# Kernel optimization log

Measured on AMD Instinct MI355X. Metric: run time of the kernel, lower is better.

## Reference

```python
import jax, jax.numpy as jnp
import numpy as np

N = 50000
E = 800000
D = 128
H = 8
HD = D // H


def setup_inputs() -> dict:
    key = jax.random.key(0)
    ks = jax.random.split(key, 12)
    s = 1.0 / np.sqrt(D)
    x = jax.random.normal(ks[0], (N, D), dtype=jnp.float32)
    edge_index = jax.random.randint(ks[1], (2, E), 0, N, dtype=jnp.int64)
    edge_bias = jax.random.normal(ks[2], (E, H), dtype=jnp.float32)
    Wq = jax.random.uniform(ks[3], (D, D), jnp.float32, -s, s)
    bq = jax.random.uniform(ks[4], (D,), jnp.float32, -s, s)
    Wk = jax.random.uniform(ks[5], (D, D), jnp.float32, -s, s)
    bk = jax.random.uniform(ks[6], (D,), jnp.float32, -s, s)
    Wv = jax.random.uniform(ks[7], (D, D), jnp.float32, -s, s)
    bv = jax.random.uniform(ks[8], (D,), jnp.float32, -s, s)
    Wo = jax.random.uniform(ks[9], (D, D), jnp.float32, -s, s)
    bo = jax.random.uniform(ks[10], (D,), jnp.float32, -s, s)
    return {"x": x, "edge_index": edge_index, "edge_bias": edge_bias,
            "Wq": Wq, "bq": bq, "Wk": Wk, "bk": bk,
            "Wv": Wv, "bv": bv, "Wo": Wo, "bo": bo}


def reference(x, edge_index, edge_bias, Wq, bq, Wk, bk, Wv, bv, Wo, bo):
    scale = HD ** -0.5
    row, col = edge_index[0], edge_index[1]
    # Node-level projections -> [N, H, HD]
    q = (x @ Wq + bq).reshape(N, H, HD)
    k = (x @ Wk + bk).reshape(N, H, HD)
    v = (x @ Wv + bv).reshape(N, H, HD)
    # Edge-level gather + per-edge attention logits [E, H]
    q_i = q[col]
    k_j = k[row]
    v_j = v[row]
    attn = jnp.einsum('ehd,ehd->eh', q_i, k_j) * scale + edge_bias
    # Scatter-softmax over incoming edges of each destination node (col)
    seg_max = jax.ops.segment_max(attn, col, num_segments=N)  # [N, H]
    seg_max = jnp.where(jnp.isfinite(seg_max), seg_max, 0.0)  # empty segments -> 0
    ex = jnp.exp(attn - seg_max[col])
    denom = jax.ops.segment_sum(ex, col, num_segments=N)      # [N, H]
    attn = ex / (denom[col] + 1e-16)
    # Scatter-add weighted values -> [N, H, HD]
    weighted_v = attn[:, :, None] * v_j
    out = jax.ops.segment_sum(weighted_v, col, num_segments=N)
    out = out.reshape(N, D)
    return out @ Wo + bo
```

## Files before the change

kernel.cpp:

```cpp
#include <hip/hip_runtime.h>
#include <math.h>

#define NN 50000
#define EE 800000
#define DD 128
#define HH 8
#define HDD 16
#define CAP 64
#define NXCD 8
#define NPG 6250
#define SL 2048
#define NSL 391
#define NSTRIP 3125
#define QB 782
#define FILLB 3128
#define LTS 130

typedef __attribute__((ext_vector_type(8))) short short8;
typedef __attribute__((ext_vector_type(4))) float f32x4;

union U8 { ushort u[8]; int4 v; short8 s; };

__device__ __forceinline__ ushort f2bf(float f) {
    uint u = __float_as_uint(f);
    uint r = (u + 0x7fffu + ((u >> 16) & 1u)) >> 16;
    return (ushort)r;
}
__device__ __forceinline__ float bf2f(ushort u) {
    return __uint_as_float(((uint)u) << 16);
}

__global__ void k_prep(const float* __restrict__ Wq, const float* __restrict__ Wk,
                       const float* __restrict__ Wv, const float* __restrict__ Wo,
                       const float* __restrict__ bq, const float* __restrict__ bk,
                       const float* __restrict__ bv, const float* __restrict__ bo,
                       ushort* __restrict__ Wt, float* __restrict__ bpack) {
    int tid = blockIdx.x * 256 + threadIdx.x;
    int w = tid >> 14, rem = tid & 16383, c = rem >> 7, i = rem & 127;
    const float* W = (w == 0) ? Wq : (w == 1) ? Wk : (w == 2) ? Wv : Wo;
    float s = (w == 0) ? 0.25f : 1.0f;
    Wt[(size_t)w * 16384 + c * 128 + i] = f2bf(W[i * 128 + c] * s);
    if (i == 0) {
        const float* B = (w == 0) ? bq : (w == 1) ? bk : (w == 2) ? bv : bo;
        bpack[w * 128 + c] = B[c] * s;
    }
}

__global__ __launch_bounds__(256) void k_pre(
    const float* __restrict__ x, const ushort* __restrict__ Wt,
    const float* __restrict__ bpk,
    ushort* __restrict__ qb, ushort* __restrict__ kk, ushort* __restrict__ vv,
    const int* __restrict__ col, const int* __restrict__ row,
    int* __restrict__ cursor, int2* __restrict__ reB) {
    __shared__ ushort T[4][16 * LTS];
    int tid = threadIdx.x;
    int b = blockIdx.x;

    if (b >= QB) {
        int fi = b - QB;
        int g = b & 7;
        int j = fi >> 3;
        int lo = g * NPG, hi = lo + NPG;
        int base = j * SL + tid * 8;
        if (base < EE) {
            int4 c0 = *(const int4*)&col[base];
            int4 c1 = *(const int4*)&col[base + 4];
            int cs[8] = {c0.x, c0.y, c0.z, c0.w, c1.x, c1.y, c1.z, c1.w};
            int lim = EE - base;
#pragma unroll
            for (int t = 0; t < 8; t++) {
                if (t < lim) {
                    int c = cs[t];
                    if (c >= lo && c < hi) {
                        int e = base + t;
                        int p = atomicAdd(&cursor[c], 1);
                        if (p < CAP) reB[(size_t)c * CAP + p] = make_int2(row[e], e);
                    }
                }
            }
        }
        return;
    }

    int wave = tid >> 6, lane = tid & 63;
    int strip = b * 4 + wave;
    if (strip >= NSTRIP) return;
    int r0 = strip * 16;
    int lr = lane & 15, lg = lane >> 4;
    ushort* Tw = T[wave];

    short8 afr[4];
    const float* xp = x + (size_t)(r0 + lr) * 128;
#pragma unroll
    for (int ks = 0; ks < 4; ks++) {
        const float* ap = xp + ks * 32 + lg * 8;
        float4 f0 = *(const float4*)ap;
        float4 f1 = *(const float4*)(ap + 4);
        U8 r;
        r.u[0] = f2bf(f0.x); r.u[1] = f2bf(f0.y); r.u[2] = f2bf(f0.z); r.u[3] = f2bf(f0.w);
        r.u[4] = f2bf(f1.x); r.u[5] = f2bf(f1.y); r.u[6] = f2bf(f1.z); r.u[7] = f2bf(f1.w);
        afr[ks] = r.s;
    }

    for (int w = 0; w < 3; w++) {
        f32x4 acc[8];
#pragma unroll
        for (int n = 0; n < 8; n++) acc[n] = (f32x4){0.f, 0.f, 0.f, 0.f};
        const ushort* Wb = Wt + (size_t)w * 16384;
#pragma unroll
        for (int ks = 0; ks < 4; ks++) {
            short8 bfr[8];
#pragma unroll
            for (int n = 0; n < 8; n++)
                bfr[n] = *(const short8*)&Wb[(n * 16 + lr) * 128 + ks * 32 + lg * 8];
#pragma unroll
            for (int n = 0; n < 8; n++)
                acc[n] = __builtin_amdgcn_mfma_f32_16x16x32_bf16(afr[ks], bfr[n], acc[n], 0, 0, 0);
        }

#pragma unroll
        for (int n = 0; n < 8; n++) {
            float bv_ = bpk[w * 128 + n * 16 + lr];
#pragma unroll
            for (int rg = 0; rg < 4; rg++)
                Tw[(lg * 4 + rg) * LTS + n * 16 + lr] = f2bf(acc[n][rg] + bv_);
        }
        ushort* dst = (w == 0) ? qb : (w == 1) ? kk : vv;
#pragma unroll
        for (int i = 0; i < 4; i++) {
            int4 vd = *(const int4*)&Tw[(i * 4 + lg) * LTS + lr * 8];
            *(int4*)&dst[(size_t)(r0 + i * 4 + lg) * 128 + lr * 8] = vd;
        }
    }
}

__global__ __launch_bounds__(256) void k_gemm_out(
    const ushort* __restrict__ A, const ushort* __restrict__ Bt,
    const float* __restrict__ bias, float* __restrict__ Cf) {
    int tid = threadIdx.x;
    int wave = tid >> 6, lane = tid & 63;
    int strip = blockIdx.x * 4 + wave;
    if (strip >= NSTRIP) return;
    int r0 = strip * 16;
    int lr = lane & 15, lg = lane >> 4;

    short8 afr[4];
#pragma unroll
    for (int ks = 0; ks < 4; ks++)
        afr[ks] = *(const short8*)&A[(size_t)(r0 + lr) * 128 + ks * 32 + lg * 8];

    f32x4 acc[8];
#pragma unroll
    for (int n = 0; n < 8; n++) acc[n] = (f32x4){0.f, 0.f, 0.f, 0.f};
#pragma unroll
    for (int ks = 0; ks < 4; ks++) {
        short8 bfr[8];
#pragma unroll
        for (int n = 0; n < 8; n++)
            bfr[n] = *(const short8*)&Bt[(n * 16 + lr) * 128 + ks * 32 + lg * 8];
#pragma unroll
        for (int n = 0; n < 8; n++)
            acc[n] = __builtin_amdgcn_mfma_f32_16x16x32_bf16(afr[ks], bfr[n], acc[n], 0, 0, 0);
    }
#pragma unroll
    for (int n = 0; n < 8; n++) {
        int gcol = n * 16 + lr;
        float bv_ = bias[gcol];
#pragma unroll
        for (int rg = 0; rg < 4; rg++) {
            int grow = r0 + lg * 4 + rg;
            Cf[(size_t)grow * 128 + gcol] = acc[n][rg] + bv_;
        }
    }
}

__global__ __launch_bounds__(256) void k_attn(
    const ushort* __restrict__ qb, const ushort* __restrict__ kk,
    const ushort* __restrict__ vv, const float* __restrict__ ebias,
    const int2* __restrict__ reB, const int* __restrict__ deg,
    ushort* __restrict__ aggb) {
    int wave = threadIdx.x >> 6;
    int lane = threadIdx.x & 63;
    int n = blockIdx.x * 4 + wave;
    if (n >= NN) return;
    int cnt = min(deg[n], CAP);
    const int2* bucket = reB + (size_t)n * CAP;
    int h = lane >> 3;
    int j = lane & 7;
    int hb = lane & ~7;

    float qf[16];
    {
        U8 q0, q1;
        const ushort* qp = qb + (size_t)n * DD + h * HDD;
        q0.v = *(const int4*)qp;
        q1.v = *(const int4*)(qp + 8);
#pragma unroll
        for (int t = 0; t < 8; t++) qf[t] = bf2f(q0.u[t]);
#pragma unroll
        for (int t = 0; t < 8; t++) qf[8 + t] = bf2f(q1.u[t]);
    }

    float m = -INFINITY;
    float denom = 0.f;
    float acc0 = 0.f, acc1 = 0.f;

    for (int idx = 0; idx < cnt; idx += 8) {
        int my = idx + j;
        bool valid = my < cnt;
        int2 re = valid ? bucket[my] : make_int2(0, 0);
        int r = re.x;
        float logit = -INFINITY;
        if (valid) {
            const ushort* kp = kk + (size_t)r * DD + h * HDD;
            U8 a0, a1;
            a0.v = *(const int4*)kp;
            a1.v = *(const int4*)(kp + 8);
            float d = 0.f;
#pragma unroll
            for (int t = 0; t < 8; t++) d += qf[t] * bf2f(a0.u[t]);
#pragma unroll
            for (int t = 0; t < 8; t++) d += qf[8 + t] * bf2f(a1.u[t]);
            logit = d + ebias[(size_t)re.y * HH + h];
        }
        float cm = logit;
        cm = fmaxf(cm, __shfl_xor(cm, 1));
        cm = fmaxf(cm, __shfl_xor(cm, 2));
        cm = fmaxf(cm, __shfl_xor(cm, 4));
        float mnew = fmaxf(m, cm);
        float sc = __expf(m - mnew);
        float p = __expf(logit - mnew);
        m = mnew;
        float ps = p;
        ps += __shfl_xor(ps, 1);
        ps += __shfl_xor(ps, 2);
        ps += __shfl_xor(ps, 4);
        denom = denom * sc + ps;
        acc0 *= sc;
        acc1 *= sc;
#pragma unroll
        for (int j2 = 0; j2 < 8; j2++) {
            float pj = __shfl(p, hb + j2);
            int rj = __shfl(r, hb + j2);
            uint vp = *(const uint*)(vv + (size_t)rj * DD + 2 * lane);
            acc0 += pj * bf2f((ushort)(vp & 0xffffu));
            acc1 += pj * bf2f((ushort)(vp >> 16));
        }
    }
    float inv = 1.0f / (denom + 1e-16f);
    uint pack = (uint)f2bf(acc0 * inv) | ((uint)f2bf(acc1 * inv) << 16);
    *(uint*)&aggb[(size_t)n * DD + 2 * lane] = pack;
}

extern "C" void kernel_launch(void* const* d_in, const int* in_sizes, int n_in,
                              void* d_out, int out_size, void* d_ws, size_t ws_size,
                              hipStream_t stream) {
    const float* x     = (const float*)d_in[0];
    const int*   eidx  = (const int*)d_in[1];
    const float* ebias = (const float*)d_in[2];
    const float* Wq    = (const float*)d_in[3];
    const float* bq    = (const float*)d_in[4];
    const float* Wk    = (const float*)d_in[5];
    const float* bk    = (const float*)d_in[6];
    const float* Wv    = (const float*)d_in[7];
    const float* bv    = (const float*)d_in[8];
    const float* Wo    = (const float*)d_in[9];
    const float* bo    = (const float*)d_in[10];
    float* out = (float*)d_out;

    const int* row = eidx;
    const int* col = eidx + EE;

    char* p = (char*)d_ws;
    ushort* qb    = (ushort*)p;  p += (size_t)NN * DD * 2;
    ushort* kk    = (ushort*)p;  p += (size_t)NN * DD * 2;
    ushort* vvp   = (ushort*)p;  p += (size_t)NN * DD * 2;
    ushort* aggb  = (ushort*)p;  p += (size_t)NN * DD * 2;
    ushort* Wt    = (ushort*)p;  p += (size_t)4 * 16384 * 2;
    float*  bpk   = (float*)p;   p += 4 * 128 * 4;
    int2*   reB   = (int2*)p;    p += (size_t)NN * CAP * 8;
    int* cursor   = (int*)p;     p += (size_t)NN * 4;

    hipMemsetAsync(cursor, 0, (size_t)NN * sizeof(int), stream);

    hipLaunchKernelGGL(k_prep, dim3(256), dim3(256), 0, stream,
                       Wq, Wk, Wv, Wo, bq, bk, bv, bo, Wt, bpk);

    hipLaunchKernelGGL(k_pre, dim3(QB + FILLB), dim3(256), 0, stream,
                       x, Wt, bpk, qb, kk, vvp, col, row, cursor, reB);

    hipLaunchKernelGGL(k_attn, dim3(NN / 4), dim3(256), 0, stream,
                       qb, kk, vvp, ebias, reB, cursor, aggb);

    hipLaunchKernelGGL(k_gemm_out, dim3((NSTRIP + 3) / 4), dim3(256), 0, stream,
                       aggb, Wt + 3 * 16384, bpk + 3 * 128, out);
}
```

Before: 178.1 us.

## Split CSR fill into two node halves and overlap with QKV and attention

Result: slower. 205.8 us (+15.5%).

```diff
diff --git a/kernel.cpp b/kernel.cpp
--- a/kernel.cpp
+++ b/kernel.cpp
@@ -7,13 +7,15 @@
 #define HH 8
 #define HDD 16
 #define CAP 64
-#define NXCD 8
-#define NPG 6250
+#define HALF 25000
+#define NPG 3125
 #define SL 2048
-#define NSL 391
 #define NSTRIP 3125
 #define QB 782
-#define FILLB 3128
+#define P1B 3910
+#define P2B 9380
+#define P3B 6250
+#define P4B 782
 #define LTS 130
 
 typedef __attribute__((ext_vector_type(8))) short short8;
@@ -30,65 +32,43 @@
     return __uint_as_float(((uint)u) << 16);
 }
 
-__global__ void k_prep(const float* __restrict__ Wq, const float* __restrict__ Wk,
-                       const float* __restrict__ Wv, const float* __restrict__ Wo,
-                       const float* __restrict__ bq, const float* __restrict__ bk,
-                       const float* __restrict__ bv, const float* __restrict__ bo,
-                       ushort* __restrict__ Wt, float* __restrict__ bpack) {
-    int tid = blockIdx.x * 256 + threadIdx.x;
-    int w = tid >> 14, rem = tid & 16383, c = rem >> 7, i = rem & 127;
-    const float* W = (w == 0) ? Wq : (w == 1) ? Wk : (w == 2) ? Wv : Wo;
-    float s = (w == 0) ? 0.25f : 1.0f;
-    Wt[(size_t)w * 16384 + c * 128 + i] = f2bf(W[i * 128 + c] * s);
-    if (i == 0) {
-        const float* B = (w == 0) ? bq : (w == 1) ? bk : (w == 2) ? bv : bo;
-        bpack[w * 128 + c] = B[c] * s;
-    }
-}
-
-__global__ __launch_bounds__(256) void k_pre(
-    const float* __restrict__ x, const ushort* __restrict__ Wt,
-    const float* __restrict__ bpk,
-    ushort* __restrict__ qb, ushort* __restrict__ kk, ushort* __restrict__ vv,
-    const int* __restrict__ col, const int* __restrict__ row,
-    int* __restrict__ cursor, int2* __restrict__ reB) {
-    __shared__ ushort T[4][16 * LTS];
-    int tid = threadIdx.x;
-    int b = blockIdx.x;
-
-    if (b >= QB) {
-        int fi = b - QB;
-        int g = b & 7;
-        int j = fi >> 3;
-        int lo = g * NPG, hi = lo + NPG;
-        int base = j * SL + tid * 8;
-        if (base < EE) {
-            int4 c0 = *(const int4*)&col[base];
-            int4 c1 = *(const int4*)&col[base + 4];
-            int cs[8] = {c0.x, c0.y, c0.z, c0.w, c1.x, c1.y, c1.z, c1.w};
-            int lim = EE - base;
-#pragma unroll
-            for (int t = 0; t < 8; t++) {
-                if (t < lim) {
-                    int c = cs[t];
-                    if (c >= lo && c < hi) {
-                        int e = base + t;
-                        int p = atomicAdd(&cursor[c], 1);
-                        if (p < CAP) reB[(size_t)c * CAP + p] = make_int2(row[e], e);
-                    }
-                }
+
+__device__ __forceinline__ void do_fill(int fi, int nbase, int tid,
+                                        const int* __restrict__ col,
+                                        const int* __restrict__ row,
+                                        int* __restrict__ cursor,
+                                        int2* __restrict__ reB) {
+    int g = fi & 7;
+    int slice = fi >> 3;
+    int lo = nbase + g * NPG, hi = lo + NPG;
+    int base = slice * SL + tid * 8;
+    if (base >= EE) return;
+    int4 c0 = *(const int4*)&col[base];
+    int4 c1 = *(const int4*)&col[base + 4];
+    int cs[8] = {c0.x, c0.y, c0.z, c0.w, c1.x, c1.y, c1.z, c1.w};
+    int lim = EE - base;
+#pragma unroll
+    for (int t = 0; t < 8; t++) {
+        if (t < lim) {
+            int c = cs[t];
+            if (c >= lo && c < hi) {
+                int e = base + t;
+                int p = atomicAdd(&cursor[c], 1);
+                if (p < CAP) reB[(size_t)c * CAP + p] = make_int2(row[e], e);
             }
         }
-        return;
-    }
-
-    int wave = tid >> 6, lane = tid & 63;
-    int strip = b * 4 + wave;
-    if (strip >= NSTRIP) return;
+    }
+}
+
+__device__ __forceinline__ void do_qkv_strip(int strip, int lane, ushort* Tw,
+                                             const float* __restrict__ x,
+                                             const ushort* __restrict__ Wt,
+                                             const float* __restrict__ bpk,
+                                             ushort* __restrict__ qb,
+                                             ushort* __restrict__ kk,
+                                             ushort* __restrict__ vv) {
     int r0 = strip * 16;
     int lr = lane & 15, lg = lane >> 4;
-    ushort* Tw = T[wave];
-
     short8 afr[4];
     const float* xp = x + (size_t)(r0 + lr) * 128;
 #pragma unroll
@@ -101,7 +81,6 @@
         r.u[4] = f2bf(f1.x); r.u[5] = f2bf(f1.y); r.u[6] = f2bf(f1.z); r.u[7] = f2bf(f1.w);
         afr[ks] = r.s;
     }
-
     for (int w = 0; w < 3; w++) {
         f32x4 acc[8];
 #pragma unroll
@@ -117,7 +96,6 @@
             for (int n = 0; n < 8; n++)
                 acc[n] = __builtin_amdgcn_mfma_f32_16x16x32_bf16(afr[ks], bfr[n], acc[n], 0, 0, 0);
         }
-
 #pragma unroll
         for (int n = 0; n < 8; n++) {
             float bv_ = bpk[w * 128 + n * 16 + lr];
@@ -134,55 +112,14 @@
     }
 }
 
-__global__ __launch_bounds__(256) void k_gemm_out(
-    const ushort* __restrict__ A, const ushort* __restrict__ Bt,
-    const float* __restrict__ bias, float* __restrict__ Cf) {
-    int tid = threadIdx.x;
-    int wave = tid >> 6, lane = tid & 63;
-    int strip = blockIdx.x * 4 + wave;
-    if (strip >= NSTRIP) return;
-    int r0 = strip * 16;
-    int lr = lane & 15, lg = lane >> 4;
-
-    short8 afr[4];
-#pragma unroll
-    for (int ks = 0; ks < 4; ks++)
-        afr[ks] = *(const short8*)&A[(size_t)(r0 + lr) * 128 + ks * 32 + lg * 8];
-
-    f32x4 acc[8];
-#pragma unroll
-    for (int n = 0; n < 8; n++) acc[n] = (f32x4){0.f, 0.f, 0.f, 0.f};
-#pragma unroll
-    for (int ks = 0; ks < 4; ks++) {
-        short8 bfr[8];
-#pragma unroll
-        for (int n = 0; n < 8; n++)
-            bfr[n] = *(const short8*)&Bt[(n * 16 + lr) * 128 + ks * 32 + lg * 8];
-#pragma unroll
-        for (int n = 0; n < 8; n++)
-            acc[n] = __builtin_amdgcn_mfma_f32_16x16x32_bf16(afr[ks], bfr[n], acc[n], 0, 0, 0);
-    }
-#pragma unroll
-    for (int n = 0; n < 8; n++) {
-        int gcol = n * 16 + lr;
-        float bv_ = bias[gcol];
-#pragma unroll
-        for (int rg = 0; rg < 4; rg++) {
-            int grow = r0 + lg * 4 + rg;
-            Cf[(size_t)grow * 128 + gcol] = acc[n][rg] + bv_;
-        }
-    }
-}
-
-__global__ __launch_bounds__(256) void k_attn(
-    const ushort* __restrict__ qb, const ushort* __restrict__ kk,
-    const ushort* __restrict__ vv, const float* __restrict__ ebias,
-    const int2* __restrict__ reB, const int* __restrict__ deg,
-    ushort* __restrict__ aggb) {
-    int wave = threadIdx.x >> 6;
-    int lane = threadIdx.x & 63;
-    int n = blockIdx.x * 4 + wave;
-    if (n >= NN) return;
+__device__ __forceinline__ void do_attn(int n, int lane,
+                                        const ushort* __restrict__ qb,
+                                        const ushort* __restrict__ kk,
+                                        const ushort* __restrict__ vv,
+                                        const float* __restrict__ ebias,
+                                        const int2* __restrict__ reB,
+                                        const int* __restrict__ deg,
+                                        ushort* __restrict__ aggb) {
     int cnt = min(deg[n], CAP);
     const int2* bucket = reB + (size_t)n * CAP;
     int h = lane >> 3;
@@ -252,6 +189,112 @@
     *(uint*)&aggb[(size_t)n * DD + 2 * lane] = pack;
 }
 
+__global__ void k_prep(const float* __restrict__ Wq, const float* __restrict__ Wk,
+                       const float* __restrict__ Wv, const float* __restrict__ Wo,
+                       const float* __restrict__ bq, const float* __restrict__ bk,
+                       const float* __restrict__ bv, const float* __restrict__ bo,
+                       ushort* __restrict__ Wt, float* __restrict__ bpack) {
+    int tid = blockIdx.x * 256 + threadIdx.x;
+    int w = tid >> 14, rem = tid & 16383, c = rem >> 7, i = rem & 127;
+    const float* W = (w == 0) ? Wq : (w == 1) ? Wk : (w == 2) ? Wv : Wo;
+    float s = (w == 0) ? 0.25f : 1.0f;
+    Wt[(size_t)w * 16384 + c * 128 + i] = f2bf(W[i * 128 + c] * s);
+    if (i == 0) {
+        const float* B = (w == 0) ? bq : (w == 1) ? bk : (w == 2) ? bv : bo;
+        bpack[w * 128 + c] = B[c] * s;
+    }
+}
+
+__global__ __launch_bounds__(256) void k_p1(
+    const float* __restrict__ x, const ushort* __restrict__ Wt,
+    const float* __restrict__ bpk,
+    ushort* __restrict__ qb, ushort* __restrict__ kk, ushort* __restrict__ vv,
+    const int* __restrict__ col, const int* __restrict__ row,
+    int* __restrict__ cursor, int2* __restrict__ reB) {
+    __shared__ ushort T[4][16 * LTS];
+    int tid = threadIdx.x;
+    int b = blockIdx.x;
+    if (b % 5 != 0) {
+        do_fill(b - b / 5 - 1, 0, tid, col, row, cursor, reB);
+        return;
+    }
+    int wave = tid >> 6, lane = tid & 63;
+    int strip = (b / 5) * 4 + wave;
+    if (strip >= NSTRIP) return;
+    do_qkv_strip(strip, lane, T[wave], x, Wt, bpk, qb, kk, vv);
+}
+
+__global__ __launch_bounds__(256) void k_p2(
+    const ushort* __restrict__ qb, const ushort* __restrict__ kk,
+    const ushort* __restrict__ vv, const float* __restrict__ ebias,
+    const int2* __restrict__ reB, const int* __restrict__ cursor,
+    ushort* __restrict__ aggb,
+    const int* __restrict__ col, const int* __restrict__ row,
+    int* __restrict__ cursor_w) {
+    int tid = threadIdx.x;
+    int b = blockIdx.x;
+    if (b >= 9378 || (b % 3) == 2) {
+        int fi = (b >= 9378) ? (3126 + (b - 9378)) : (b / 3);
+        do_fill(fi, HALF, tid, col, row, cursor_w, (int2*)reB);
+        return;
+    }
+    int ai = b - (b + 1) / 3;
+    if (ai >= HALF / 4) return;
+    int wave = tid >> 6, lane = tid & 63;
+    int n = ai * 4 + wave;
+    do_attn(n, lane, qb, kk, vv, ebias, reB, cursor, aggb);
+}
+
+__global__ __launch_bounds__(256) void k_p3(
+    const ushort* __restrict__ qb, const ushort* __restrict__ kk,
+    const ushort* __restrict__ vv, const float* __restrict__ ebias,
+    const int2* __restrict__ reB, const int* __restrict__ cursor,
+    ushort* __restrict__ aggb) {
+    int wave = threadIdx.x >> 6, lane = threadIdx.x & 63;
+    int n = HALF + blockIdx.x * 4 + wave;
+    do_attn(n, lane, qb, kk, vv, ebias, reB, cursor, aggb);
+}
+
+__global__ __launch_bounds__(256) void k_p4(
+    const ushort* __restrict__ A, const ushort* __restrict__ Bt,
+    const float* __restrict__ bias, float* __restrict__ Cf) {
+    int tid = threadIdx.x;
+    int wave = tid >> 6, lane = tid & 63;
+    int strip = blockIdx.x * 4 + wave;
+    if (strip >= NSTRIP) return;
+    int r0 = strip * 16;
+    int lr = lane & 15, lg = lane >> 4;
+
+    short8 afr[4];
+#pragma unroll
+    for (int ks = 0; ks < 4; ks++)
+        afr[ks] = *(const short8*)&A[(size_t)(r0 + lr) * 128 + ks * 32 + lg * 8];
+
+    f32x4 acc[8];
+#pragma unroll
+    for (int n = 0; n < 8; n++) acc[n] = (f32x4){0.f, 0.f, 0.f, 0.f};
+#pragma unroll
+    for (int ks = 0; ks < 4; ks++) {
+        short8 bfr[8];
+#pragma unroll
+        for (int n = 0; n < 8; n++)
+            bfr[n] = *(const short8*)&Bt[(n * 16 + lr) * 128 + ks * 32 + lg * 8];
+#pragma unroll
+        for (int n = 0; n < 8; n++)
+            acc[n] = __builtin_amdgcn_mfma_f32_16x16x32_bf16(afr[ks], bfr[n], acc[n], 0, 0, 0);
+    }
+#pragma unroll
+    for (int n = 0; n < 8; n++) {
+        int gcol = n * 16 + lr;
+        float bv_ = bias[gcol];
+#pragma unroll
+        for (int rg = 0; rg < 4; rg++) {
+            int grow = r0 + lg * 4 + rg;
+            Cf[(size_t)grow * 128 + gcol] = acc[n][rg] + bv_;
+        }
+    }
+}
+
 extern "C" void kernel_launch(void* const* d_in, const int* in_sizes, int n_in,
                               void* d_out, int out_size, void* d_ws, size_t ws_size,
                               hipStream_t stream) {
@@ -286,12 +329,15 @@
     hipLaunchKernelGGL(k_prep, dim3(256), dim3(256), 0, stream,
                        Wq, Wk, Wv, Wo, bq, bk, bv, bo, Wt, bpk);
 
-    hipLaunchKernelGGL(k_pre, dim3(QB + FILLB), dim3(256), 0, stream,
+    hipLaunchKernelGGL(k_p1, dim3(P1B), dim3(256), 0, stream,
                        x, Wt, bpk, qb, kk, vvp, col, row, cursor, reB);
 
-    hipLaunchKernelGGL(k_attn, dim3(NN / 4), dim3(256), 0, stream,
+    hipLaunchKernelGGL(k_p2, dim3(P2B), dim3(256), 0, stream,
+                       qb, kk, vvp, ebias, reB, cursor, aggb, col, row, cursor);
+
+    hipLaunchKernelGGL(k_p3, dim3(P3B), dim3(256), 0, stream,
                        qb, kk, vvp, ebias, reB, cursor, aggb);
 
-    hipLaunchKernelGGL(k_gemm_out, dim3((NSTRIP + 3) / 4), dim3(256), 0, stream,
+    hipLaunchKernelGGL(k_p4, dim3(P4B), dim3(256), 0, stream,
                        aggb, Wt + 3 * 16384, bpk + 3 * 128, out);
 }
```
